# Optimization experiments

Measured on AMD Instinct MI355X. Metric: run time of the kernel, lower is better.

## Reference

```python
import jax, jax.numpy as jnp
import numpy as np

N_NODES = 100000
N_EDGES = 500000
IN_FEATS = 128
HID = 128
OUT = 1


def setup_inputs() -> dict:
    key = jax.random.key(0)
    ks = jax.random.split(key, 10)
    h = jax.random.normal(ks[0], (N_NODES, IN_FEATS), dtype=jnp.float32)
    src = jax.random.randint(ks[1], (N_EDGES,), 0, N_NODES, dtype=jnp.int32)
    dst = jax.random.randint(ks[2], (N_EDGES,), 0, N_NODES, dtype=jnp.int32)
    # Linear params (PyTorch convention: W [out,in], y = x @ W.T + b)
    s1 = 1.0 / np.sqrt(2 * IN_FEATS)
    s2 = 1.0 / np.sqrt(HID)
    W1 = jax.random.uniform(ks[3], (HID, 2 * IN_FEATS), jnp.float32, -s1, s1)
    b1 = jax.random.uniform(ks[4], (HID,), jnp.float32, -s1, s1)
    W2 = jax.random.uniform(ks[5], (HID, HID), jnp.float32, -s2, s2)
    b2 = jax.random.uniform(ks[6], (HID,), jnp.float32, -s2, s2)
    W3 = jax.random.uniform(ks[7], (OUT, HID), jnp.float32, -s2, s2)
    b3 = jax.random.uniform(ks[8], (OUT,), jnp.float32, -s2, s2)
    return {"h": h, "src": src, "dst": dst,
            "W1": W1, "b1": b1, "W2": W2, "b2": b2, "W3": W3, "b3": b3}


def reference(h, src, dst, W1, b1, W2, b2, W3, b3):
    # Per-edge gather of src/dst node features. Instead of materializing the
    # [E, 2*in] concat, split W1 into its src/dst halves and fuse the concat
    # into two GEMMs (same math as fc1(cat([h_u, h_v], 1))).
    h_u = h[src]                                   # [E, in]
    h_v = h[dst]                                   # [E, in]
    W1u, W1v = W1[:, :IN_FEATS], W1[:, IN_FEATS:]  # [hid, in] each
    x = h_u @ W1u.T + h_v @ W1v.T + b1             # [E, hid]
    x = jax.nn.relu(x)
    x = jax.nn.relu(x @ W2.T + b2)                 # [E, hid]
    score = x @ W3.T + b3                          # [E, out]
    return score
```

## Files before the change

### kernel.cpp

```cpp
#include <hip/hip_runtime.h>
#include <hip/hip_bf16.h>
#include <hip/hip_fp16.h>


#define N_NODES 100000
#define N_EDGES 500000
#define F       128
#define HID     128
#define TE      64
#define NT      ((N_EDGES + TE - 1) / TE)
#define GRID    256
#define BLOCK   512

typedef _Float16 f16x8  __attribute__((ext_vector_type(8)));
typedef float    f32x16 __attribute__((ext_vector_type(16)));

typedef __attribute__((address_space(3))) unsigned int  lds_u32;
typedef __attribute__((address_space(1))) const unsigned int glb_u32;

__device__ __forceinline__ void load_lds16(const void* g, void* l) {
    __builtin_amdgcn_global_load_lds((glb_u32*)g, (lds_u32*)l, 16, 0, 0);
}
__device__ __forceinline__ void bar_lgkm() {
    asm volatile("s_waitcnt lgkmcnt(0)" ::: "memory");
    __builtin_amdgcn_s_barrier();
    __builtin_amdgcn_sched_barrier(0);
}
__device__ __forceinline__ void bar_vm() {
    asm volatile("s_waitcnt vmcnt(0) lgkmcnt(0)" ::: "memory");
    __builtin_amdgcn_s_barrier();
    __builtin_amdgcn_sched_barrier(0);
}

__global__ __launch_bounds__(256) void h_to_f16(const float* __restrict__ h,
                                                _Float16* __restrict__ h16) {
    const int i = (blockIdx.x * 256 + threadIdx.x) * 8;
    float4 a = *(const float4*)(h + i);
    float4 b = *(const float4*)(h + i + 4);
    f16x8 v;
    v[0] = (_Float16)a.x; v[1] = (_Float16)a.y; v[2] = (_Float16)a.z; v[3] = (_Float16)a.w;
    v[4] = (_Float16)b.x; v[5] = (_Float16)b.y; v[6] = (_Float16)b.z; v[7] = (_Float16)b.w;
    *(f16x8*)(h16 + i) = v;
}

__global__ __launch_bounds__(BLOCK, 2) void edge_mlp_v3(
    const _Float16* __restrict__ h16,
    const int*   __restrict__ src,
    const int*   __restrict__ dst,
    const float* __restrict__ W1,
    const float* __restrict__ b1,
    const float* __restrict__ W2,
    const float* __restrict__ b2,
    const float* __restrict__ W3,
    const float* __restrict__ b3,
    float*       __restrict__ out)
{
    __shared__ __align__(128) char Alds[2 * TE * 512];
    __shared__ __align__(128) char Xlds[TE * 256];
    __shared__ float Spart[8][32];

    const int tid  = threadIdx.x;
    const int wave = tid >> 6;
    const int lane = tid & 63;
    const int mh   = wave >> 1;
    const int ne   = wave & 1;
    const int col  = lane & 31;
    const int h    = lane >> 5;

    f16x8 w1a[16];
    #pragma unroll
    for (int kt = 0; kt < 16; ++kt) {
        const float* p = W1 + (mh * 32 + col) * 256 + kt * 16 + 8 * h;
        f16x8 v;
        #pragma unroll
        for (int j = 0; j < 8; ++j) v[j] = (_Float16)p[j];
        w1a[kt] = v;
    }
    f16x8 w2a[8];
    #pragma unroll
    for (int kt = 0; kt < 8; ++kt) {
        const float* p = W2 + (mh * 32 + col) * 128 + kt * 16 + 8 * h;
        f16x8 v;
        #pragma unroll
        for (int j = 0; j < 8; ++j) v[j] = (_Float16)p[j];
        w2a[kt] = v;
    }
    float b1pl[16], b2pl[16], w3pl[16];
    #pragma unroll
    for (int r = 0; r < 16; ++r) {
        const int row = mh * 32 + (r & 3) + 8 * (r >> 2) + 4 * h;
        b1pl[r] = b1[row];
        b2pl[r] = b2[row];
        w3pl[r] = W3[row];
    }
    const float b3v = b3[0];

    int eloc[4], k16v[4];
    #pragma unroll
    for (int j = 0; j < 4; ++j) {
        const int i = wave * 4 + j;
        eloc[j] = 2 * i + h;
        k16v[j] = (lane & 15) ^ (eloc[j] & 15);
    }
    const int whichv = (lane >> 4) & 1;
    const int* idxp  = whichv ? dst : src;

    const int t0 = blockIdx.x;
    int nodeCur[4], nodeNext[4];

    #pragma unroll
    for (int j = 0; j < 4; ++j) {
        int eg = t0 * TE + eloc[j];
        if (eg >= N_EDGES) eg = N_EDGES - 1;
        nodeCur[j] = idxp[eg];
    }
    #pragma unroll
    for (int j = 0; j < 4; ++j) {
        const _Float16* g = h16 + (size_t)nodeCur[j] * F + k16v[j] * 8;
        load_lds16(g, Alds + (wave * 4 + j) * 1024);
    }
    {
        int tn = t0 + GRID; if (tn > NT - 1) tn = NT - 1;
        #pragma unroll
        for (int j = 0; j < 4; ++j) {
            int eg = tn * TE + eloc[j];
            if (eg >= N_EDGES) eg = N_EDGES - 1;
            nodeNext[j] = idxp[eg];
        }
    }

    const int e_own = ne * 32 + col;
    const int exor  = (e_own & 15) << 4;

    int cur = 0;
    for (int t = t0; t < NT; t += GRID) {
        bar_vm();

        #pragma unroll
        for (int j = 0; j < 4; ++j) nodeCur[j] = nodeNext[j];
        {
            char* nb = Alds + (cur ^ 1) * (TE * 512);
            #pragma unroll
            for (int j = 0; j < 4; ++j) {
                const _Float16* g = h16 + (size_t)nodeCur[j] * F + k16v[j] * 8;
                load_lds16(g, nb + (wave * 4 + j) * 1024);
            }
        }
        {
            int tn2 = t + 2 * GRID; if (tn2 > NT - 1) tn2 = NT - 1;
            #pragma unroll
            for (int j = 0; j < 4; ++j) {
                int eg = tn2 * TE + eloc[j];
                if (eg >= N_EDGES) eg = N_EDGES - 1;
                nodeNext[j] = idxp[eg];
            }
        }

        const char* Ab = Alds + cur * (TE * 512);

        f32x16 acc1 = {};
        #pragma unroll
        for (int kt = 0; kt < 16; ++kt) {
            const int c = (kt * 32 + 16 * h) ^ exor;
            f16x8 bf = *(const f16x8*)(Ab + e_own * 512 + c);
            acc1 = __builtin_amdgcn_mfma_f32_32x32x16_f16(w1a[kt], bf, acc1, 0, 0, 0);
        }
        #pragma unroll
        for (int pr = 0; pr < 8; ++pr) {
            float v0 = acc1[2 * pr]     + b1pl[2 * pr];
            float v1 = acc1[2 * pr + 1] + b1pl[2 * pr + 1];
            v0 = v0 > 0.f ? v0 : 0.f;
            v1 = v1 > 0.f ? v1 : 0.f;
            union { _Float16 q[2]; unsigned u; } pk;
            pk.q[0] = (_Float16)v0; pk.q[1] = (_Float16)v1;
            const int row0 = mh * 32 + ((2 * pr) & 3) + 8 * (pr >> 1) + 4 * h;
            const int c = (row0 * 2) ^ exor;
            *(unsigned*)(Xlds + e_own * 256 + c) = pk.u;
        }
        bar_lgkm();

        f32x16 acc2 = {};
        #pragma unroll
        for (int kt = 0; kt < 8; ++kt) {
            const int c = (kt * 32 + 16 * h) ^ exor;
            f16x8 xf = *(const f16x8*)(Xlds + e_own * 256 + c);
            acc2 = __builtin_amdgcn_mfma_f32_32x32x16_f16(w2a[kt], xf, acc2, 0, 0, 0);
        }

        float p = 0.f;
        #pragma unroll
        for (int r = 0; r < 16; ++r) {
            float v = acc2[r] + b2pl[r];
            v = v > 0.f ? v : 0.f;
            p = fmaf(w3pl[r], v, p);
        }
        p += __shfl_xor(p, 32);
        if (lane < 32) Spart[wave][lane] = p;
        bar_lgkm();

        if (tid < TE) {
            const int eg = t * TE + tid;
            const int w0 = tid >> 5, c0 = tid & 31;
            float s = Spart[w0][c0] + Spart[2 + w0][c0]
                    + Spart[4 + w0][c0] + Spart[6 + w0][c0] + b3v;
            if (eg < N_EDGES) out[eg] = s;
        }
        cur ^= 1;
    }
}

__global__ __launch_bounds__(512) void edge_mlp_v1(
    const float* __restrict__ h,
    const int*   __restrict__ src,
    const int*   __restrict__ dst,
    const float* __restrict__ W1,
    const float* __restrict__ b1,
    const float* __restrict__ W2,
    const float* __restrict__ b2,
    const float* __restrict__ W3,
    const float* __restrict__ b3,
    float*       __restrict__ out)
{
    __shared__ __align__(128) char Alds[TE * 512];
    __shared__ __align__(128) char Xlds[TE * 256];
    typedef float f32x4 __attribute__((ext_vector_type(4)));

    const int tid  = threadIdx.x;
    const int wave = tid >> 6;
    const int lane = tid & 63;
    const int l15  = lane & 15;
    const int lk   = lane >> 4;
    const int n1 = wave * 16 + l15;

    f16x8 w1f[8];
    #pragma unroll
    for (int kt = 0; kt < 8; ++kt) {
        const float* p = W1 + n1 * 256 + kt * 32 + lk * 8;
        f16x8 v;
        #pragma unroll
        for (int j = 0; j < 8; ++j) v[j] = (_Float16)p[j];
        w1f[kt] = v;
    }
    const float b1v = b1[n1];
    f16x8 w2f[4];
    #pragma unroll
    for (int kt = 0; kt < 4; ++kt) {
        const float* p = W2 + n1 * 128 + kt * 32 + lk * 8;
        f16x8 v;
        #pragma unroll
        for (int j = 0; j < 8; ++j) v[j] = (_Float16)p[j];
        w2f[kt] = v;
    }
    const float b2v = b2[n1];
    float w3r[16];
    {
        const float* p = W3 + (tid & 7) * 16;
        #pragma unroll
        for (int i = 0; i < 16; ++i) w3r[i] = p[i];
    }
    const float b3v = b3[0];

    const int slot = tid >> 2, part = tid & 3;
    const int g_e = slot >> 1, g_which = slot & 1;

    for (int t = blockIdx.x; t < NT; t += gridDim.x) {
        {
            int eg = t * TE + g_e;
            if (eg >= N_EDGES) eg = N_EDGES - 1;
            const int node = g_which ? dst[eg] : src[eg];
            const float* p = h + node * F + part * 32;
            const int kbase = g_which * 128 + part * 32;
            #pragma unroll
            for (int c = 0; c < 4; ++c) {
                float4 v0 = *(const float4*)(p + c * 8);
                float4 v1 = *(const float4*)(p + c * 8 + 4);
                f16x8 x;
                x[0] = (_Float16)v0.x; x[1] = (_Float16)v0.y;
                x[2] = (_Float16)v0.z; x[3] = (_Float16)v0.w;
                x[4] = (_Float16)v1.x; x[5] = (_Float16)v1.y;
                x[6] = (_Float16)v1.z; x[7] = (_Float16)v1.w;
                int byte = g_e * 512 + (kbase + c * 8) * 2;
                byte ^= (g_e & 7) << 4;
                *(f16x8*)(Alds + byte) = x;
            }
        }
        __syncthreads();
        #pragma unroll
        for (int m = 0; m < 4; ++m) {
            f32x4 acc = {0.f, 0.f, 0.f, 0.f};
            #pragma unroll
            for (int kt = 0; kt < 8; ++kt) {
                const int edge = m * 16 + l15;
                int byte = edge * 512 + (kt * 32 + lk * 8) * 2;
                byte ^= (edge & 7) << 4;
                f16x8 a = *(const f16x8*)(Alds + byte);
                acc = __builtin_amdgcn_mfma_f32_16x16x32_f16(a, w1f[kt], acc, 0, 0, 0);
            }
            #pragma unroll
            for (int r = 0; r < 4; ++r) {
                float v = acc[r] + b1v;
                v = v > 0.f ? v : 0.f;
                const int edge = m * 16 + lk * 4 + r;
                int byte = edge * 256 + n1 * 2;
                byte ^= (edge & 7) << 4;
                *(_Float16*)(Xlds + byte) = (_Float16)v;
            }
        }
        __syncthreads();
        f32x4 acc2[4];
        #pragma unroll
        for (int m = 0; m < 4; ++m) {
            f32x4 acc = {0.f, 0.f, 0.f, 0.f};
            #pragma unroll
            for (int kt = 0; kt < 4; ++kt) {
                const int edge = m * 16 + l15;
                int byte = edge * 256 + (kt * 32 + lk * 8) * 2;
                byte ^= (edge & 7) << 4;
                f16x8 a = *(const f16x8*)(Xlds + byte);
                acc = __builtin_amdgcn_mfma_f32_16x16x32_f16(a, w2f[kt], acc, 0, 0, 0);
            }
            acc2[m] = acc;
        }
        __syncthreads();
        #pragma unroll
        for (int m = 0; m < 4; ++m) {
            #pragma unroll
            for (int r = 0; r < 4; ++r) {
                float v = acc2[m][r] + b2v;
                v = v > 0.f ? v : 0.f;
                const int edge = m * 16 + lk * 4 + r;
                int byte = edge * 256 + n1 * 2;
                byte ^= (edge & 7) << 4;
                *(_Float16*)(Xlds + byte) = (_Float16)v;
            }
        }
        __syncthreads();
        {
            const int e_loc = tid >> 3;
            const int cgrp  = tid & 7;
            const int swz   = (e_loc & 7) << 4;
            const int base  = e_loc * 256 + cgrp * 32;
            f16x8 x0 = *(const f16x8*)(Xlds + (base ^ swz));
            f16x8 x1 = *(const f16x8*)(Xlds + ((base + 16) ^ swz));
            float p = 0.f;
            #pragma unroll
            for (int i = 0; i < 8; ++i) p += (float)x0[i] * w3r[i];
            #pragma unroll
            for (int i = 0; i < 8; ++i) p += (float)x1[i] * w3r[8 + i];
            p += __shfl_xor(p, 1);
            p += __shfl_xor(p, 2);
            p += __shfl_xor(p, 4);
            const int eg = t * TE + e_loc;
            if (cgrp == 0 && eg < N_EDGES) out[eg] = p + b3v;
        }
    }
}

extern "C" void kernel_launch(void* const* d_in, const int* in_sizes, int n_in,
                              void* d_out, int out_size, void* d_ws, size_t ws_size,
                              hipStream_t stream) {
    const float* h   = (const float*)d_in[0];
    const int*   src = (const int*)  d_in[1];
    const int*   dst = (const int*)  d_in[2];
    const float* W1  = (const float*)d_in[3];
    const float* b1  = (const float*)d_in[4];
    const float* W2  = (const float*)d_in[5];
    const float* b2  = (const float*)d_in[6];
    const float* W3  = (const float*)d_in[7];
    const float* b3  = (const float*)d_in[8];
    float* out = (float*)d_out;

    const size_t need = (size_t)N_NODES * F * sizeof(_Float16);
    if (ws_size >= need) {
        _Float16* h16 = (_Float16*)d_ws;
        h_to_f16<<<6250, 256, 0, stream>>>(h, h16);
        edge_mlp_v3<<<GRID, BLOCK, 0, stream>>>(h16, src, dst, W1, b1, W2, b2, W3, b3, out);
    } else {
        edge_mlp_v1<<<512, 512, 0, stream>>>(h, src, dst, W1, b1, W2, b2, W3, b3, out);
    }
}
```

Baseline: 184.6 us.

## Shrink edge tile to 32 with 256-thread blocks and reuse X buffer for partials

Halves the edge tile to 32 edges and the block to four waves, each wave owning 32 hidden rows for all edges, with a 1024-block grid and four blocks per CU requested. The partial-sum buffer now aliases the X staging buffer (an extra barrier is added), layer-1 results are stored as 64-bit packed groups instead of 32-bit pairs, and edge-bounds clamping is dropped because 500000 divides evenly by 32. The aim is higher occupancy and smaller LDS per block so more tiles are in flight to hide gather latency, at the cost of an extra barrier per tile and weights re-held in registers by more blocks.

Result: slower. 348.7 us (+88.8%).

```diff
diff --git a/kernel.cpp b/kernel.cpp
--- a/kernel.cpp
+++ b/kernel.cpp
@@ -7,10 +7,10 @@
 #define N_EDGES 500000
 #define F       128
 #define HID     128
-#define TE      64
-#define NT      ((N_EDGES + TE - 1) / TE)
-#define GRID    256
-#define BLOCK   512
+#define TE      32
+#define NT      (N_EDGES / TE)
+#define GRID    1024
+#define BLOCK   256
 
 typedef _Float16 f16x8  __attribute__((ext_vector_type(8)));
 typedef float    f32x16 __attribute__((ext_vector_type(16)));
@@ -43,7 +43,7 @@
     *(f16x8*)(h16 + i) = v;
 }
 
-__global__ __launch_bounds__(BLOCK, 2) void edge_mlp_v3(
+__global__ __launch_bounds__(BLOCK, 4) void edge_mlp_v4(
     const _Float16* __restrict__ h16,
     const int*   __restrict__ src,
     const int*   __restrict__ dst,
@@ -57,13 +57,12 @@
 {
     __shared__ __align__(128) char Alds[2 * TE * 512];
     __shared__ __align__(128) char Xlds[TE * 256];
-    __shared__ float Spart[8][32];
+    float* Spart = (float*)Xlds;
 
     const int tid  = threadIdx.x;
     const int wave = tid >> 6;
     const int lane = tid & 63;
-    const int mh   = wave >> 1;
-    const int ne   = wave & 1;
+    const int mh   = wave;
     const int col  = lane & 31;
     const int h    = lane >> 5;
 
@@ -110,9 +109,7 @@
 
     #pragma unroll
     for (int j = 0; j < 4; ++j) {
-        int eg = t0 * TE + eloc[j];
-        if (eg >= N_EDGES) eg = N_EDGES - 1;
-        nodeCur[j] = idxp[eg];
+        nodeCur[j] = idxp[t0 * TE + eloc[j]];
     }
     #pragma unroll
     for (int j = 0; j < 4; ++j) {
@@ -122,14 +119,10 @@
     {
         int tn = t0 + GRID; if (tn > NT - 1) tn = NT - 1;
         #pragma unroll
-        for (int j = 0; j < 4; ++j) {
-            int eg = tn * TE + eloc[j];
-            if (eg >= N_EDGES) eg = N_EDGES - 1;
-            nodeNext[j] = idxp[eg];
-        }
-    }
-
-    const int e_own = ne * 32 + col;
+        for (int j = 0; j < 4; ++j) nodeNext[j] = idxp[tn * TE + eloc[j]];
+    }
+
+    const int e_own = col;
     const int exor  = (e_own & 15) << 4;
 
     int cur = 0;
@@ -149,11 +142,7 @@
         {
             int tn2 = t + 2 * GRID; if (tn2 > NT - 1) tn2 = NT - 1;
             #pragma unroll
-            for (int j = 0; j < 4; ++j) {
-                int eg = tn2 * TE + eloc[j];
-                if (eg >= N_EDGES) eg = N_EDGES - 1;
-                nodeNext[j] = idxp[eg];
-            }
+            for (int j = 0; j < 4; ++j) nodeNext[j] = idxp[tn2 * TE + eloc[j]];
         }
 
         const char* Ab = Alds + cur * (TE * 512);
@@ -166,16 +155,16 @@
             acc1 = __builtin_amdgcn_mfma_f32_32x32x16_f16(w1a[kt], bf, acc1, 0, 0, 0);
         }
         #pragma unroll
-        for (int pr = 0; pr < 8; ++pr) {
-            float v0 = acc1[2 * pr]     + b1pl[2 * pr];
-            float v1 = acc1[2 * pr + 1] + b1pl[2 * pr + 1];
-            v0 = v0 > 0.f ? v0 : 0.f;
-            v1 = v1 > 0.f ? v1 : 0.f;
-            union { _Float16 q[2]; unsigned u; } pk;
-            pk.q[0] = (_Float16)v0; pk.q[1] = (_Float16)v1;
-            const int row0 = mh * 32 + ((2 * pr) & 3) + 8 * (pr >> 1) + 4 * h;
-            const int c = (row0 * 2) ^ exor;
-            *(unsigned*)(Xlds + e_own * 256 + c) = pk.u;
+        for (int g = 0; g < 4; ++g) {
+            union { _Float16 q[4]; unsigned long long u; } pk;
+            #pragma unroll
+            for (int q = 0; q < 4; ++q) {
+                float v = acc1[4 * g + q] + b1pl[4 * g + q];
+                v = v > 0.f ? v : 0.f;
+                pk.q[q] = (_Float16)v;
+            }
+            const int c = (mh * 64 + 16 * g + 8 * h) ^ exor;
+            *(unsigned long long*)(Xlds + e_own * 256 + c) = pk.u;
         }
         bar_lgkm();
 
@@ -195,15 +184,15 @@
             p = fmaf(w3pl[r], v, p);
         }
         p += __shfl_xor(p, 32);
-        if (lane < 32) Spart[wave][lane] = p;
+
         bar_lgkm();
+        if (lane < 32) Spart[wave * 32 + lane] = p;
+        bar_lgkm();
 
         if (tid < TE) {
-            const int eg = t * TE + tid;
-            const int w0 = tid >> 5, c0 = tid & 31;
-            float s = Spart[w0][c0] + Spart[2 + w0][c0]
-                    + Spart[4 + w0][c0] + Spart[6 + w0][c0] + b3v;
-            if (eg < N_EDGES) out[eg] = s;
+            float s = Spart[tid] + Spart[32 + tid] + Spart[64 + tid]
+                    + Spart[96 + tid] + b3v;
+            out[t * TE + tid] = s;
         }
         cur ^= 1;
     }
@@ -221,8 +210,8 @@
     const float* __restrict__ b3,
     float*       __restrict__ out)
 {
-    __shared__ __align__(128) char Alds[TE * 512];
-    __shared__ __align__(128) char Xlds[TE * 256];
+    __shared__ __align__(128) char Alds[64 * 512];
+    __shared__ __align__(128) char Xlds[64 * 256];
     typedef float f32x4 __attribute__((ext_vector_type(4)));
 
     const int tid  = threadIdx.x;
@@ -231,6 +220,7 @@
     const int l15  = lane & 15;
     const int lk   = lane >> 4;
     const int n1 = wave * 16 + l15;
+    const int NT1 = (N_EDGES + 63) / 64;
 
     f16x8 w1f[8];
     #pragma unroll
@@ -263,9 +253,9 @@
     const int slot = tid >> 2, part = tid & 3;
     const int g_e = slot >> 1, g_which = slot & 1;
 
-    for (int t = blockIdx.x; t < NT; t += gridDim.x) {
+    for (int t = blockIdx.x; t < NT1; t += gridDim.x) {
         {
-            int eg = t * TE + g_e;
+            int eg = t * 64 + g_e;
             if (eg >= N_EDGES) eg = N_EDGES - 1;
             const int node = g_which ? dst[eg] : src[eg];
             const float* p = h + node * F + part * 32;
@@ -350,7 +340,7 @@
             p += __shfl_xor(p, 1);
             p += __shfl_xor(p, 2);
             p += __shfl_xor(p, 4);
-            const int eg = t * TE + e_loc;
+            const int eg = t * 64 + e_loc;
             if (cgrp == 0 && eg < N_EDGES) out[eg] = p + b3v;
         }
     }
@@ -374,7 +364,7 @@
     if (ws_size >= need) {
         _Float16* h16 = (_Float16*)d_ws;
         h_to_f16<<<6250, 256, 0, stream>>>(h, h16);
-        edge_mlp_v3<<<GRID, BLOCK, 0, stream>>>(h16, src, dst, W1, b1, W2, b2, W3, b3, out);
+        edge_mlp_v4<<<GRID, BLOCK, 0, stream>>>(h16, src, dst, W1, b1, W2, b2, W3, b3, out);
     } else {
         edge_mlp_v1<<<512, 512, 0, stream>>>(h, src, dst, W1, b1, W2, b2, W3, b3, out);
     }
```
